# Performance work log

Measured on AMD Instinct MI355X. Metric: run time of the kernel, lower is better.

The kernel has to match this reference:

```python
import jax, jax.numpy as jnp
import numpy as np

N, D, NUM_IDS = 4096, 2048, 256
MARGIN = 0.3


def _pairwise_euclidean(x):
    # torch.cdist(x, x, p=2): safe sqrt of squared distances (zero-grad at 0)
    sq = jnp.sum(x * x, axis=1)                      # [N]
    d2 = sq[:, None] + sq[None, :] - 2.0 * (x @ x.T)  # [N, N]
    d2 = jnp.maximum(d2, 0.0)
    d = jnp.sqrt(jnp.where(d2 > 0.0, d2, 1.0))
    return jnp.where(d2 > 0.0, d, 0.0)


def setup_inputs() -> dict:
    key = jax.random.key(0)
    k1, k2 = jax.random.split(key)
    features = jax.random.normal(k1, (N, D), dtype=jnp.float32)
    labels = jax.random.randint(k2, (N,), 0, NUM_IDS, dtype=jnp.int64)
    return {"features": features, "labels": labels}


def reference(features, labels):
    dist = _pairwise_euclidean(features)                     # [N, N]
    mask_pos = labels[None, :] == labels[:, None]            # [N, N] bool
    # batch-hard mining: hardest positive (max), hardest negative (min)
    dist_ap = jnp.max(jnp.where(mask_pos, dist, 0.0), axis=1)       # [N]
    dist_an = jnp.min(jnp.where(mask_pos, jnp.inf, dist), axis=1)   # [N]
    valid = (dist_ap > 0.0) & jnp.isfinite(dist_an)
    # MarginRankingLoss(dist_an, dist_ap, y=1) = mean(relu(dist_ap - dist_an + margin))
    per_anchor = jnp.maximum(dist_ap - dist_an + MARGIN, 0.0)
    n_valid = jnp.sum(valid)
    loss = jnp.sum(jnp.where(valid, per_anchor, 0.0)) / jnp.maximum(n_valid, 1).astype(per_anchor.dtype)
    return jnp.where(n_valid > 0, loss, 0.0)
```

## Files before the change

kernel.cpp:

```cpp
#include <hip/hip_runtime.h>

#define NN 4096
#define DD 2048
#define MARGIN_F 0.3f
#define NTILES 1056
#define BK 128
#define NIT (DD / BK)
#define QS (127.0f / 6.0f)
#define C2 (2.0f * (6.0f / 127.0f) * (6.0f / 127.0f))

typedef __attribute__((ext_vector_type(4))) int i32x4;

__device__ __forceinline__ unsigned q8(float v) {
    int i = __float2int_rn(v * QS);
    i = min(127, max(-127, i));
    return (unsigned)(i & 255);
}

__global__ __launch_bounds__(256) void prep_kernel(const float* __restrict__ x,
                                                   unsigned char* __restrict__ xq,
                                                   float* __restrict__ sq,
                                                   unsigned int* __restrict__ ap,
                                                   unsigned int* __restrict__ an,
                                                   int* __restrict__ counter) {
    const int wave = threadIdx.x >> 6, lane = threadIdx.x & 63;
    const int row = blockIdx.x * 4 + wave;
    const float* xr = x + (size_t)row * DD;
    unsigned int* orow = (unsigned int*)(xq + (size_t)row * DD);
    float s = 0.0f;
#pragma unroll
    for (int j = 0; j < 8; ++j) {
        float4 v = ((const float4*)xr)[j * 64 + lane];
        s += v.x * v.x + v.y * v.y + v.z * v.z + v.w * v.w;
        orow[j * 64 + lane] = q8(v.x) | (q8(v.y) << 8) | (q8(v.z) << 16) | (q8(v.w) << 24);
    }
    for (int off = 32; off > 0; off >>= 1) s += __shfl_down(s, off, 64);
    if (lane == 0) {
        sq[row] = s;
        ap[row] = 0u;
        an[row] = 0x7F800000u;
    }
    if (threadIdx.x == 0 && blockIdx.x == 0) counter[0] = 0;
}

__global__ __launch_bounds__(256) void gemm_reduce_kernel(
    const unsigned char* __restrict__ xq,
    const float* __restrict__ sq,
    const int* __restrict__ labels,
    unsigned int* __restrict__ ap,
    unsigned int* __restrict__ an,
    int* __restrict__ counter,
    float* __restrict__ out) {
    __shared__ __align__(16) unsigned char As[64 * BK];
    __shared__ __align__(16) unsigned char Bs[128 * BK];

    int rem = blockIdx.x;
    int mi64 = 0;
    while (rem >= 32 - (mi64 >> 1)) { rem -= 32 - (mi64 >> 1); ++mi64; }
    const int nj = (mi64 >> 1) + rem;
    const int row0 = mi64 * 64;
    const int col0 = nj * 128;
    const int phase = (blockIdx.x & 7) * 2;

    const int t = threadIdx.x;
    const int lane = t & 63;
    const int wave = t >> 6;
    const int c = lane & 15;
    const int q = lane >> 4;
    const int wc = wave * 32;

    i32x4 acc[4][2];
#pragma unroll
    for (int mi = 0; mi < 4; ++mi)
#pragma unroll
        for (int ni = 0; ni < 2; ++ni)
            acc[mi][ni] = (i32x4){0, 0, 0, 0};

    const int rowb = t >> 3;
    const int colsw = (t & 7) ^ (rowb & 7);
    const unsigned char* gA[2];
    const unsigned char* gB[4];
#pragma unroll
    for (int s = 0; s < 2; ++s)
        gA[s] = xq + (size_t)(row0 + rowb + 32 * s) * DD + colsw * 16;
#pragma unroll
    for (int s = 0; s < 4; ++s)
        gB[s] = xq + (size_t)(col0 + rowb + 32 * s) * DD + colsw * 16;

    for (int it = 0; it < NIT; ++it) {
        const int k0 = ((it + phase) & (NIT - 1)) * BK;
#pragma unroll
        for (int s = 0; s < 2; ++s)
            __builtin_amdgcn_global_load_lds(
                (const __attribute__((address_space(1))) void*)(gA[s] + k0),
                (__attribute__((address_space(3))) void*)&As[(t + 256 * s) * 16],
                16, 0, 0);
#pragma unroll
        for (int s = 0; s < 4; ++s)
            __builtin_amdgcn_global_load_lds(
                (const __attribute__((address_space(1))) void*)(gB[s] + k0),
                (__attribute__((address_space(3))) void*)&Bs[(t + 256 * s) * 16],
                16, 0, 0);
        __syncthreads();

        const i32x4* Av = (const i32x4*)As;
        const i32x4* Bv = (const i32x4*)Bs;
#pragma unroll
        for (int ks = 0; ks < 2; ++ks) {
            const int kc = q + 4 * ks;
            i32x4 af[4], bfr[2];
#pragma unroll
            for (int mi = 0; mi < 4; ++mi) {
                const int r = mi * 16 + c;
                af[mi] = Av[r * 8 + (kc ^ (r & 7))];
            }
#pragma unroll
            for (int ni = 0; ni < 2; ++ni) {
                const int r = wc + ni * 16 + c;
                bfr[ni] = Bv[r * 8 + (kc ^ (r & 7))];
            }
#pragma unroll
            for (int mi = 0; mi < 4; ++mi)
#pragma unroll
                for (int ni = 0; ni < 2; ++ni)
                    acc[mi][ni] = __builtin_amdgcn_mfma_i32_16x16x64_i8(
                        af[mi], bfr[ni], acc[mi][ni], 0, 0, 0);
        }
        __syncthreads();
    }

    float sq_col[2];
    int lab_col[2];
#pragma unroll
    for (int ni = 0; ni < 2; ++ni) {
        const int gj = col0 + wc + ni * 16 + c;
        sq_col[ni] = sq[gj];
        lab_col[ni] = labels[gj];
    }
    int lab_row[4][4];
    float dist[4][2][4];
#pragma unroll
    for (int mi = 0; mi < 4; ++mi) {
#pragma unroll
        for (int r = 0; r < 4; ++r) {
            const int gi = row0 + mi * 16 + q * 4 + r;
            const float sqi = sq[gi];
            lab_row[mi][r] = labels[gi];
#pragma unroll
            for (int ni = 0; ni < 2; ++ni) {
                float d2 = sqi + sq_col[ni] - C2 * (float)acc[mi][ni][r];
                dist[mi][ni][r] = sqrtf(fmaxf(d2, 0.0f));
            }
        }
    }

#pragma unroll
    for (int mi = 0; mi < 4; ++mi) {
#pragma unroll
        for (int r = 0; r < 4; ++r) {
            const int gi = row0 + mi * 16 + q * 4 + r;
            const int li = lab_row[mi][r];
            float apm = 0.0f;
            float anm = __builtin_inff();
#pragma unroll
            for (int ni = 0; ni < 2; ++ni) {
                const int gj = col0 + wc + ni * 16 + c;
                const float d = dist[mi][ni][r];
                if (li == lab_col[ni]) {
                    if (gi != gj) apm = fmaxf(apm, d);
                } else {
                    anm = fminf(anm, d);
                }
            }
#pragma unroll
            for (int off = 1; off < 16; off <<= 1) {
                apm = fmaxf(apm, __shfl_xor(apm, off, 16));
                anm = fminf(anm, __shfl_xor(anm, off, 16));
            }
            if (c == 0) {
                atomicMax(&ap[gi], __float_as_uint(apm));
                atomicMin(&an[gi], __float_as_uint(anm));
            }
        }
    }

#pragma unroll
    for (int ni = 0; ni < 2; ++ni) {
        const int gj = col0 + wc + ni * 16 + c;
        const int lj = lab_col[ni];
        float apm = 0.0f;
        float anm = __builtin_inff();
#pragma unroll
        for (int mi = 0; mi < 4; ++mi) {
#pragma unroll
            for (int r = 0; r < 4; ++r) {
                const int gi = row0 + mi * 16 + q * 4 + r;
                const float d = dist[mi][ni][r];
                if (lj == lab_row[mi][r]) {
                    if (gi != gj) apm = fmaxf(apm, d);
                } else {
                    anm = fminf(anm, d);
                }
            }
        }
        apm = fmaxf(apm, __shfl_xor(apm, 16, 64));
        anm = fminf(anm, __shfl_xor(anm, 16, 64));
        apm = fmaxf(apm, __shfl_xor(apm, 32, 64));
        anm = fminf(anm, __shfl_xor(anm, 32, 64));
        if (q == 0) {
            atomicMax(&ap[gj], __float_as_uint(apm));
            atomicMin(&an[gj], __float_as_uint(anm));
        }
    }

    __syncthreads();
    int* flag = (int*)As;
    if (t == 0) {
        int old = __hip_atomic_fetch_add(counter, 1, __ATOMIC_ACQ_REL,
                                         __HIP_MEMORY_SCOPE_AGENT);
        flag[0] = (old == NTILES - 1) ? 1 : 0;
    }
    __syncthreads();
    if (flag[0]) {
        float sum = 0.0f;
        int cnt = 0;
        for (int i = t; i < NN; i += 256) {
            const float a = __uint_as_float(__hip_atomic_load(
                &ap[i], __ATOMIC_RELAXED, __HIP_MEMORY_SCOPE_AGENT));
            const float b = __uint_as_float(__hip_atomic_load(
                &an[i], __ATOMIC_RELAXED, __HIP_MEMORY_SCOPE_AGENT));
            if ((a > 0.0f) && (b < __builtin_inff())) {
                sum += fmaxf(a - b + MARGIN_F, 0.0f);
                cnt += 1;
            }
        }
        for (int off = 32; off > 0; off >>= 1) {
            sum += __shfl_down(sum, off, 64);
            cnt += __shfl_down(cnt, off, 64);
        }
        float* ssum = (float*)Bs;
        int* scnt = (int*)Bs + 8;
        if (lane == 0) { ssum[wave] = sum; scnt[wave] = cnt; }
        __syncthreads();
        if (t == 0) {
            float s = 0.0f; int n = 0;
#pragma unroll
            for (int w = 0; w < 4; ++w) { s += ssum[w]; n += scnt[w]; }
            out[0] = (n > 0) ? s / (float)n : 0.0f;
        }
    }
}

extern "C" void kernel_launch(void* const* d_in, const int* in_sizes, int n_in,
                              void* d_out, int out_size, void* d_ws, size_t ws_size,
                              hipStream_t stream) {
    const float* x = (const float*)d_in[0];
    const int* labels = (const int*)d_in[1];
    float* out = (float*)d_out;

    char* ws = (char*)d_ws;
    unsigned char* xq = (unsigned char*)ws;
    float* sq = (float*)(ws + (size_t)NN * DD);
    unsigned int* ap = (unsigned int*)(ws + (size_t)NN * DD + (size_t)NN * 4);
    unsigned int* an = (unsigned int*)(ws + (size_t)NN * DD + (size_t)NN * 8);
    int* counter = (int*)(ws + (size_t)NN * DD + (size_t)NN * 12);

    prep_kernel<<<NN / 4, 256, 0, stream>>>(x, xq, sq, ap, an, counter);
    gemm_reduce_kernel<<<NTILES, 256, 0, stream>>>(xq, sq, labels, ap, an, counter, out);
}
```

Before: 143.1 us.

## Replace LDS-staged block GEMM with per-wave 64x64 tiles loading directly from global

The shared-memory staged 64x128 block tiling is replaced by independent per-wave 64x64 upper-triangular tiles. Each wave loads its int8 MFMA fragments straight from global memory and runs a fully unrolled K loop, with no LDS and no barriers. The intent is to remove LDS staging and synchronisation overhead and to raise occupancy with launch_bounds(256,2). The cost is that operand reuse across waves now depends on L1/L2 caching rather than shared memory, and the load pattern (16 rows × 64 bytes per instruction) may be less coalesced.

```diff
diff --git a/kernel.cpp b/kernel.cpp
--- a/kernel.cpp
+++ b/kernel.cpp
@@ -3,9 +3,8 @@
 #define NN 4096
 #define DD 2048
 #define MARGIN_F 0.3f
-#define NTILES 1056
-#define BK 128
-#define NIT (DD / BK)
+#define NWT 2080
+#define NBLK 520
 #define QS (127.0f / 6.0f)
 #define C2 (2.0f * (6.0f / 127.0f) * (6.0f / 127.0f))
 
@@ -43,7 +42,7 @@
     if (threadIdx.x == 0 && blockIdx.x == 0) counter[0] = 0;
 }
 
-__global__ __launch_bounds__(256) void gemm_reduce_kernel(
+__global__ __launch_bounds__(256, 2) void gemm_reduce_kernel(
     const unsigned char* __restrict__ xq,
     const float* __restrict__ sq,
     const int* __restrict__ labels,
@@ -51,94 +50,67 @@
     unsigned int* __restrict__ an,
     int* __restrict__ counter,
     float* __restrict__ out) {
-    __shared__ __align__(16) unsigned char As[64 * BK];
-    __shared__ __align__(16) unsigned char Bs[128 * BK];
-
-    int rem = blockIdx.x;
-    int mi64 = 0;
-    while (rem >= 32 - (mi64 >> 1)) { rem -= 32 - (mi64 >> 1); ++mi64; }
-    const int nj = (mi64 >> 1) + rem;
-    const int row0 = mi64 * 64;
-    const int col0 = nj * 128;
-    const int phase = (blockIdx.x & 7) * 2;
+    __shared__ float ssum[4];
+    __shared__ int scnt[4];
+    __shared__ int flag;
 
     const int t = threadIdx.x;
     const int lane = t & 63;
     const int wave = t >> 6;
     const int c = lane & 15;
     const int q = lane >> 4;
-    const int wc = wave * 32;
-
-    i32x4 acc[4][2];
+
+    const int wid = blockIdx.x * 4 + wave;
+    int rem = wid;
+    int ti = 0;
+    while (rem >= 64 - ti) { rem -= 64 - ti; ++ti; }
+    const int tj = ti + rem;
+    const int row0 = ti * 64;
+    const int col0 = tj * 64;
+
+    const unsigned char* pA[4];
+    const unsigned char* pB[4];
 #pragma unroll
     for (int mi = 0; mi < 4; ++mi)
-#pragma unroll
-        for (int ni = 0; ni < 2; ++ni)
-            acc[mi][ni] = (i32x4){0, 0, 0, 0};
-
-    const int rowb = t >> 3;
-    const int colsw = (t & 7) ^ (rowb & 7);
-    const unsigned char* gA[2];
-    const unsigned char* gB[4];
-#pragma unroll
-    for (int s = 0; s < 2; ++s)
-        gA[s] = xq + (size_t)(row0 + rowb + 32 * s) * DD + colsw * 16;
-#pragma unroll
-    for (int s = 0; s < 4; ++s)
-        gB[s] = xq + (size_t)(col0 + rowb + 32 * s) * DD + colsw * 16;
-
-    for (int it = 0; it < NIT; ++it) {
-        const int k0 = ((it + phase) & (NIT - 1)) * BK;
-#pragma unroll
-        for (int s = 0; s < 2; ++s)
-            __builtin_amdgcn_global_load_lds(
-                (const __attribute__((address_space(1))) void*)(gA[s] + k0),
-                (__attribute__((address_space(3))) void*)&As[(t + 256 * s) * 16],
-                16, 0, 0);
-#pragma unroll
-        for (int s = 0; s < 4; ++s)
-            __builtin_amdgcn_global_load_lds(
-                (const __attribute__((address_space(1))) void*)(gB[s] + k0),
-                (__attribute__((address_space(3))) void*)&Bs[(t + 256 * s) * 16],
-                16, 0, 0);
-        __syncthreads();
-
-        const i32x4* Av = (const i32x4*)As;
-        const i32x4* Bv = (const i32x4*)Bs;
-#pragma unroll
-        for (int ks = 0; ks < 2; ++ks) {
-            const int kc = q + 4 * ks;
-            i32x4 af[4], bfr[2];
-#pragma unroll
-            for (int mi = 0; mi < 4; ++mi) {
-                const int r = mi * 16 + c;
-                af[mi] = Av[r * 8 + (kc ^ (r & 7))];
-            }
-#pragma unroll
-            for (int ni = 0; ni < 2; ++ni) {
-                const int r = wc + ni * 16 + c;
-                bfr[ni] = Bv[r * 8 + (kc ^ (r & 7))];
-            }
-#pragma unroll
-            for (int mi = 0; mi < 4; ++mi)
-#pragma unroll
-                for (int ni = 0; ni < 2; ++ni)
-                    acc[mi][ni] = __builtin_amdgcn_mfma_i32_16x16x64_i8(
-                        af[mi], bfr[ni], acc[mi][ni], 0, 0, 0);
-        }
-        __syncthreads();
-    }
-
-    float sq_col[2];
-    int lab_col[2];
-#pragma unroll
-    for (int ni = 0; ni < 2; ++ni) {
-        const int gj = col0 + wc + ni * 16 + c;
-        sq_col[ni] = sq[gj];
-        lab_col[ni] = labels[gj];
+        pA[mi] = xq + (size_t)(row0 + mi * 16 + c) * DD + q * 16;
+#pragma unroll
+    for (int nj = 0; nj < 4; ++nj)
+        pB[nj] = xq + (size_t)(col0 + nj * 16 + c) * DD + q * 16;
+
+    i32x4 acc[4][4];
+#pragma unroll
+    for (int mi = 0; mi < 4; ++mi)
+#pragma unroll
+        for (int nj = 0; nj < 4; ++nj)
+            acc[mi][nj] = (i32x4){0, 0, 0, 0};
+
+#pragma unroll
+    for (int kc = 0; kc < 32; ++kc) {
+        i32x4 af[4], bf[4];
+#pragma unroll
+        for (int mi = 0; mi < 4; ++mi)
+            af[mi] = *(const i32x4*)(pA[mi] + (kc << 6));
+#pragma unroll
+        for (int nj = 0; nj < 4; ++nj)
+            bf[nj] = *(const i32x4*)(pB[nj] + (kc << 6));
+#pragma unroll
+        for (int mi = 0; mi < 4; ++mi)
+#pragma unroll
+            for (int nj = 0; nj < 4; ++nj)
+                acc[mi][nj] = __builtin_amdgcn_mfma_i32_16x16x64_i8(
+                    af[mi], bf[nj], acc[mi][nj], 0, 0, 0);
+    }
+
+    float sq_col[4];
+    int lab_col[4];
+#pragma unroll
+    for (int nj = 0; nj < 4; ++nj) {
+        const int gj = col0 + nj * 16 + c;
+        sq_col[nj] = sq[gj];
+        lab_col[nj] = labels[gj];
     }
     int lab_row[4][4];
-    float dist[4][2][4];
+    float dist[4][4][4];
 #pragma unroll
     for (int mi = 0; mi < 4; ++mi) {
 #pragma unroll
@@ -147,9 +119,9 @@
             const float sqi = sq[gi];
             lab_row[mi][r] = labels[gi];
 #pragma unroll
-            for (int ni = 0; ni < 2; ++ni) {
-                float d2 = sqi + sq_col[ni] - C2 * (float)acc[mi][ni][r];
-                dist[mi][ni][r] = sqrtf(fmaxf(d2, 0.0f));
+            for (int nj = 0; nj < 4; ++nj) {
+                float d2 = sqi + sq_col[nj] - C2 * (float)acc[mi][nj][r];
+                dist[mi][nj][r] = sqrtf(fmaxf(d2, 0.0f));
             }
         }
     }
@@ -163,10 +135,10 @@
             float apm = 0.0f;
             float anm = __builtin_inff();
 #pragma unroll
-            for (int ni = 0; ni < 2; ++ni) {
-                const int gj = col0 + wc + ni * 16 + c;
-                const float d = dist[mi][ni][r];
-                if (li == lab_col[ni]) {
+            for (int nj = 0; nj < 4; ++nj) {
+                const int gj = col0 + nj * 16 + c;
+                const float d = dist[mi][nj][r];
+                if (li == lab_col[nj]) {
                     if (gi != gj) apm = fmaxf(apm, d);
                 } else {
                     anm = fminf(anm, d);
@@ -185,9 +157,9 @@
     }
 
 #pragma unroll
-    for (int ni = 0; ni < 2; ++ni) {
-        const int gj = col0 + wc + ni * 16 + c;
-        const int lj = lab_col[ni];
+    for (int nj = 0; nj < 4; ++nj) {
+        const int gj = col0 + nj * 16 + c;
+        const int lj = lab_col[nj];
         float apm = 0.0f;
         float anm = __builtin_inff();
 #pragma unroll
@@ -195,7 +167,7 @@
 #pragma unroll
             for (int r = 0; r < 4; ++r) {
                 const int gi = row0 + mi * 16 + q * 4 + r;
-                const float d = dist[mi][ni][r];
+                const float d = dist[mi][nj][r];
                 if (lj == lab_row[mi][r]) {
                     if (gi != gj) apm = fmaxf(apm, d);
                 } else {
@@ -214,14 +186,13 @@
     }
 
     __syncthreads();
-    int* flag = (int*)As;
     if (t == 0) {
         int old = __hip_atomic_fetch_add(counter, 1, __ATOMIC_ACQ_REL,
                                          __HIP_MEMORY_SCOPE_AGENT);
-        flag[0] = (old == NTILES - 1) ? 1 : 0;
+        flag = (old == NBLK - 1) ? 1 : 0;
     }
     __syncthreads();
-    if (flag[0]) {
+    if (flag) {
         float sum = 0.0f;
         int cnt = 0;
         for (int i = t; i < NN; i += 256) {
@@ -238,8 +209,6 @@
             sum += __shfl_down(sum, off, 64);
             cnt += __shfl_down(cnt, off, 64);
         }
-        float* ssum = (float*)Bs;
-        int* scnt = (int*)Bs + 8;
         if (lane == 0) { ssum[wave] = sum; scnt[wave] = cnt; }
         __syncthreads();
         if (t == 0) {
@@ -266,5 +235,5 @@
     int* counter = (int*)(ws + (size_t)NN * DD + (size_t)NN * 12);
 
     prep_kernel<<<NN / 4, 256, 0, stream>>>(x, xq, sq, ap, an, counter);
-    gemm_reduce_kernel<<<NTILES, 256, 0, stream>>>(xq, sq, labels, ap, an, counter, out);
-}
+    gemm_reduce_kernel<<<NBLK, 256, 0, stream>>>(xq, sq, labels, ap, an, counter, out);
+}
```

After: 180.9 us. 26.4% more time.

## Enlarge GEMM tile to 128x128 with grouped L2-friendly tile ordering

Applied to the files above, without the earlier changes.

Each block now computes a 128x128 tile of the symmetric distance matrix instead of 64x128, which halves the number of blocks (528 upper-triangle tiles). Each B fragment loaded from LDS is reused across twice as many MFMAs, and the A fragment is loaded inside the loop to limit register pressure. A new block-index mapping spreads blocks over 8 groups and walks 4x4 super-tiles so that nearby blocks share rows and columns in cache. The cost is more accumulator and epilogue registers (launch bounds ask for 3 blocks per CU), twice the LDS per block, and fewer blocks to balance across the CUs.

```diff
diff --git a/kernel.cpp b/kernel.cpp
--- a/kernel.cpp
+++ b/kernel.cpp
@@ -3,7 +3,7 @@
 #define NN 4096
 #define DD 2048
 #define MARGIN_F 0.3f
-#define NTILES 1056
+#define NTILES 528
 #define BK 128
 #define NIT (DD / BK)
 #define QS (127.0f / 6.0f)
@@ -43,7 +43,7 @@
     if (threadIdx.x == 0 && blockIdx.x == 0) counter[0] = 0;
 }
 
-__global__ __launch_bounds__(256) void gemm_reduce_kernel(
+__global__ __launch_bounds__(256, 3) void gemm_reduce_kernel(
     const unsigned char* __restrict__ xq,
     const float* __restrict__ sq,
     const int* __restrict__ labels,
@@ -51,16 +51,29 @@
     unsigned int* __restrict__ an,
     int* __restrict__ counter,
     float* __restrict__ out) {
-    __shared__ __align__(16) unsigned char As[64 * BK];
+    __shared__ __align__(16) unsigned char As[128 * BK];
     __shared__ __align__(16) unsigned char Bs[128 * BK];
 
-    int rem = blockIdx.x;
-    int mi64 = 0;
-    while (rem >= 32 - (mi64 >> 1)) { rem -= 32 - (mi64 >> 1); ++mi64; }
-    const int nj = (mi64 >> 1) + rem;
-    const int row0 = mi64 * 64;
+    const int orig = blockIdx.x;
+    int g = (orig & 7) * (NTILES / 8) + (orig >> 3);
+    int si = 0, row_cnt = 122;
+    while (g >= row_cnt) { g -= row_cnt; ++si; row_cnt -= 16; }
+    int mi_t, nj;
+    if (g < 10) {
+        int ml = 0;
+        while (g >= 4 - ml) { g -= 4 - ml; ++ml; }
+        mi_t = si * 4 + ml;
+        nj = si * 4 + ml + g;
+    } else {
+        g -= 10;
+        const int sj = si + 1 + (g >> 4);
+        const int r = g & 15;
+        mi_t = si * 4 + (r >> 2);
+        nj = sj * 4 + (r & 3);
+    }
+    const int row0 = mi_t * 128;
     const int col0 = nj * 128;
-    const int phase = (blockIdx.x & 7) * 2;
+    const int phase = (orig & 7) * 2;
 
     const int t = threadIdx.x;
     const int lane = t & 63;
@@ -69,28 +82,27 @@
     const int q = lane >> 4;
     const int wc = wave * 32;
 
-    i32x4 acc[4][2];
-#pragma unroll
-    for (int mi = 0; mi < 4; ++mi)
+    i32x4 acc[8][2];
+#pragma unroll
+    for (int mi = 0; mi < 8; ++mi)
 #pragma unroll
         for (int ni = 0; ni < 2; ++ni)
             acc[mi][ni] = (i32x4){0, 0, 0, 0};
 
     const int rowb = t >> 3;
     const int colsw = (t & 7) ^ (rowb & 7);
-    const unsigned char* gA[2];
+    const unsigned char* gA[4];
     const unsigned char* gB[4];
 #pragma unroll
-    for (int s = 0; s < 2; ++s)
+    for (int s = 0; s < 4; ++s) {
         gA[s] = xq + (size_t)(row0 + rowb + 32 * s) * DD + colsw * 16;
-#pragma unroll
-    for (int s = 0; s < 4; ++s)
         gB[s] = xq + (size_t)(col0 + rowb + 32 * s) * DD + colsw * 16;
+    }
 
     for (int it = 0; it < NIT; ++it) {
         const int k0 = ((it + phase) & (NIT - 1)) * BK;
 #pragma unroll
-        for (int s = 0; s < 2; ++s)
+        for (int s = 0; s < 4; ++s)
             __builtin_amdgcn_global_load_lds(
                 (const __attribute__((address_space(1))) void*)(gA[s] + k0),
                 (__attribute__((address_space(3))) void*)&As[(t + 256 * s) * 16],
@@ -108,23 +120,21 @@
 #pragma unroll
         for (int ks = 0; ks < 2; ++ks) {
             const int kc = q + 4 * ks;
-            i32x4 af[4], bfr[2];
-#pragma unroll
-            for (int mi = 0; mi < 4; ++mi) {
-                const int r = mi * 16 + c;
-                af[mi] = Av[r * 8 + (kc ^ (r & 7))];
-            }
+            i32x4 bfr[2];
 #pragma unroll
             for (int ni = 0; ni < 2; ++ni) {
                 const int r = wc + ni * 16 + c;
                 bfr[ni] = Bv[r * 8 + (kc ^ (r & 7))];
             }
 #pragma unroll
-            for (int mi = 0; mi < 4; ++mi)
+            for (int mi = 0; mi < 8; ++mi) {
+                const int r = mi * 16 + c;
+                const i32x4 af = Av[r * 8 + (kc ^ (r & 7))];
 #pragma unroll
                 for (int ni = 0; ni < 2; ++ni)
                     acc[mi][ni] = __builtin_amdgcn_mfma_i32_16x16x64_i8(
-                        af[mi], bfr[ni], acc[mi][ni], 0, 0, 0);
+                        af, bfr[ni], acc[mi][ni], 0, 0, 0);
+            }
         }
         __syncthreads();
     }
@@ -137,10 +147,10 @@
         sq_col[ni] = sq[gj];
         lab_col[ni] = labels[gj];
     }
-    int lab_row[4][4];
-    float dist[4][2][4];
-#pragma unroll
-    for (int mi = 0; mi < 4; ++mi) {
+    int lab_row[8][4];
+    float dist[8][2][4];
+#pragma unroll
+    for (int mi = 0; mi < 8; ++mi) {
 #pragma unroll
         for (int r = 0; r < 4; ++r) {
             const int gi = row0 + mi * 16 + q * 4 + r;
@@ -155,7 +165,7 @@
     }
 
 #pragma unroll
-    for (int mi = 0; mi < 4; ++mi) {
+    for (int mi = 0; mi < 8; ++mi) {
 #pragma unroll
         for (int r = 0; r < 4; ++r) {
             const int gi = row0 + mi * 16 + q * 4 + r;
@@ -191,7 +201,7 @@
         float apm = 0.0f;
         float anm = __builtin_inff();
 #pragma unroll
-        for (int mi = 0; mi < 4; ++mi) {
+        for (int mi = 0; mi < 8; ++mi) {
 #pragma unroll
             for (int r = 0; r < 4; ++r) {
                 const int gi = row0 + mi * 16 + q * 4 + r;
```

Result: faster. 131.9 us, median of 2 (-7.9%).
